# Optimization experiments

Hardware: AMD Instinct MI355X
Metric: run time of the kernel (lower is better)

## Reference

```python
import jax, jax.numpy as jnp
import numpy as np

NEG_INF = -1.0e9
LEAKY_SLOPE = 0.2


def setup_inputs() -> dict:
    key = jax.random.key(0)
    k1, k2, k3, k4, k5 = jax.random.split(key, 5)
    B, N, IN, F, H = 4, 2048, 128, 64, 4
    h = jax.random.normal(k1, (B, N, IN), dtype=jnp.float32)
    adj_matrix = jax.random.randint(k2, (B, N, N), 0, 2, dtype=jnp.int32)
    W = jax.random.normal(k3, (IN, F * H), dtype=jnp.float32) * 0.05
    a1 = jax.random.normal(k4, (F,), dtype=jnp.float32) * 0.05
    a2 = jax.random.normal(k5, (F,), dtype=jnp.float32) * 0.05
    return {"h": h, "adj_matrix": adj_matrix, "W": W, "a1": a1, "a2": a2}


def reference(h, adj_matrix, W, a1, a2):
    B, N, _ = h.shape
    F = a1.shape[0]
    H = W.shape[1] // F
    # g: [B, H, N, F]
    g = (h @ W).reshape(B, N, H, F).transpose(0, 2, 1, 3)
    # additive attention split: e[p, q] = leakyrelu(a1 . g_q + a2 . g_p)
    s_dst = jnp.einsum("bhnf,f->bhn", g, a1)  # indexed by q (column)
    s_src = jnp.einsum("bhnf,f->bhn", g, a2)  # indexed by p (row)
    e = s_src[:, :, :, None] + s_dst[:, :, None, :]  # [B,H,N,N]
    e = jnp.where(e >= 0, e, LEAKY_SLOPE * e)
    e = jnp.where(adj_matrix[:, None, :, :] == 0, NEG_INF, e)
    attention = jax.nn.softmax(e, axis=-1)  # [B,H,N,N]
    # dropout omitted (deterministic/eval reference)
    h_prime = jnp.einsum("bhpq,bhqf->bpf", attention, g) / H  # mean over heads
    return h_prime, attention.mean(axis=1)
```

## Files before the change

### kernel.cpp

```cpp
#include <hip/hip_runtime.h>
#include <stdint.h>


typedef unsigned char u8;
typedef unsigned short u16;
typedef unsigned int u32;
typedef unsigned long long u64;

typedef float f32x4 __attribute__((ext_vector_type(4)));
typedef short s16x8 __attribute__((ext_vector_type(8)));
typedef u32 u32x4 __attribute__((ext_vector_type(4)));

#define B_ 4
#define N_ 2048
#define IN_ 128
#define F_ 64
#define H_ 4
#define QS_ 8

__device__ __forceinline__ float bf2f(u16 b) {
    u32 u = ((u32)b) << 16;
    return __builtin_bit_cast(float, u);
}
__device__ __forceinline__ u16 f2bf(float f) {
    u32 u = __builtin_bit_cast(u32, f);
    u += 0x7FFFu + ((u >> 16) & 1u);
    return (u16)(u >> 16);
}

__global__ __launch_bounds__(256) void kd_detect(const u32* __restrict__ hw,
                                                 u32* __restrict__ flag) {
    __shared__ int cnt[4];
    int t = threadIdx.x;
    u32 w = hw[t];
    int e0 = (int)((w >> 7) & 0xFFu);
    int sane = (e0 >= 100 && e0 <= 145) ? 1 : 0;
#pragma unroll
    for (int m = 1; m < 64; m <<= 1) sane += __shfl_xor(sane, m, 64);
    if ((t & 63) == 0) cnt[t >> 6] = sane;
    __syncthreads();
    if (t == 0) {
        int s = cnt[0] + cnt[1] + cnt[2] + cnt[3];
        *flag = (s >= 128) ? 1u : 0u;
    }
}

__device__ __forceinline__ u16 conv_elem(const void* p, int i, u32 isbf) {
    if (isbf) return ((const u16*)p)[i];
    return f2bf(((const float*)p)[i]);
}
__global__ __launch_bounds__(256) void kc_convert(
    const void* __restrict__ h, const void* __restrict__ W, const void* __restrict__ a1,
    const void* __restrict__ a2, const u32* __restrict__ flag, u16* __restrict__ hc,
    u16* __restrict__ wt, u16* __restrict__ a1c, u16* __restrict__ a2c) {
    u32 isbf = *flag;
    int idx = blockIdx.x * 256 + threadIdx.x;
    const int NH = B_ * N_ * IN_;
    if (idx < NH) {
        hc[idx] = conv_elem(h, idx, isbf);
        return;
    }
    int j = idx - NH;
    if (j < IN_ * 256) {
        int k = j >> 8, c = j & 255;
        wt[c * IN_ + k] = conv_elem(W, j, isbf);
        return;
    }
    j -= IN_ * 256;
    if (j < F_) {
        a1c[j] = conv_elem(a1, j, isbf);
        return;
    }
    j -= F_;
    if (j < F_) a2c[j] = conv_elem(a2, j, isbf);
}

__global__ __launch_bounds__(256) void k1_proj(
    const u16* __restrict__ h, const u16* __restrict__ Wt,
    const u16* __restrict__ a1, const u16* __restrict__ a2,
    u16* __restrict__ g_f, u16* __restrict__ sdb, u32* __restrict__ e2pn,
    float* __restrict__ ssA, float2* __restrict__ ssE) {
    int b = blockIdx.x >> 7;
    int n0 = (blockIdx.x & 127) * 16;
    int w = threadIdx.x >> 6;
    int lane = threadIdx.x & 63;
    int quad = lane >> 4, l15 = lane & 15;

    f32x4 acc[4];
#pragma unroll
    for (int i = 0; i < 4; i++) acc[i] = 0.0f;

    s16x8 A[4];
#pragma unroll
    for (int kt = 0; kt < 4; kt++) {
        const s16x8* ap =
            (const s16x8*)(h + ((size_t)(b * N_ + n0 + l15) * IN_ + kt * 32 + quad * 8));
        A[kt] = *ap;
    }
#pragma unroll
    for (int kt = 0; kt < 4; kt++) {
#pragma unroll
        for (int ft = 0; ft < 4; ft++) {
            int c = w * 64 + ft * 16 + l15;
            const s16x8* bp = (const s16x8*)(Wt + ((size_t)c * IN_ + kt * 32 + quad * 8));
            acc[ft] = __builtin_amdgcn_mfma_f32_16x16x32_bf16(A[kt], *bp, acc[ft], 0, 0, 0);
        }
    }
    __shared__ float ct[4][64][20];
#pragma unroll
    for (int ft = 0; ft < 4; ft++)
#pragma unroll
        for (int r = 0; r < 4; r++) ct[w][ft * 16 + l15][quad * 4 + r] = acc[ft][r];
    __syncthreads();

    float v[16];
#pragma unroll
    for (int n = 0; n < 16; n++) v[n] = ct[w][lane][n];

    {
        int chunk = n0 >> 5;
        int gq0 = (n0 >> 3) & 2;
#pragma unroll
        for (int p = 0; p < 2; p++) {
            int ft = p * 2 + (lane >> 5);
            int lq = (lane >> 4) & 1;
            int fl = lane & 15;
            s16x8 tv;
#pragma unroll
            for (int j = 0; j < 8; j++) tv[j] = (short)f2bf(ct[w][ft * 16 + fl][lq * 8 + j]);
            size_t off =
                ((size_t)(((b * H_ + w) * 4 + ft) * 64 + chunk) * 64 + (gq0 + lq) * 16 + fl) * 8;
            *(s16x8*)(g_f + off) = tv;
        }
    }
    float a1v = bf2f(a1[lane]);
    float a2v = bf2f(a2[lane]);
    float sdv = 0.f, ssv = 0.f;
#pragma unroll
    for (int n = 0; n < 16; n++) {
        float x = v[n] * a1v;
        float y = v[n] * a2v;
#pragma unroll
        for (int m = 1; m < 64; m <<= 1) {
            x += __shfl_xor(x, m, 64);
            y += __shfl_xor(y, m, 64);
        }
        if (lane == n) { sdv = x; ssv = y; }
    }
    if (lane < 16) {
        size_t o = (size_t)(b * H_ + w) * N_ + n0 + lane;
        sdb[o] = f2bf(sdv);
        float e2p = __expf(sdv), e2n = __expf(0.2f * sdv);
        e2pn[o] = (((u32)f2bf(e2p)) << 16) | (u32)f2bf(e2n);
        ssA[o] = ssv;
        ssE[o] = make_float2(__expf(ssv), __expf(0.2f * ssv));
    }
}

__global__ __launch_bounds__(256) void k2a_rowsum(
    const int* __restrict__ adj, const u16* __restrict__ sdb, const u32* __restrict__ e2pn,
    const float* __restrict__ ssA, const float2* __restrict__ ssE,
    float2* __restrict__ E1, u32* __restrict__ pk32) {
    int b = blockIdx.x >> 9;
    int p0 = (blockIdx.x & 511) * 4;
    int t = threadIdx.x;
    int w = t >> 6, lane = t & 63;

    __shared__ u8 nib[4][512];

    float tau[4][4];
#pragma unroll
    for (int r = 0; r < 4; r++)
#pragma unroll
        for (int hh = 0; hh < 4; hh++)
            tau[r][hh] = -ssA[(size_t)(b * H_ + hh) * N_ + p0 + r];

    float S[32];
#pragma unroll
    for (int i = 0; i < 32; i++) S[i] = 0.f;

#pragma unroll
    for (int i = 0; i < 2; i++) {
        int qi = i * 256 + t;
        int q = qi * 4;
        float af[4][4];
#pragma unroll
        for (int r = 0; r < 4; r++) {
            int4 av = *(const int4*)(adj + (size_t)(b * N_ + p0 + r) * N_ + q);
            af[r][0] = (av.x != 0) ? 1.f : 0.f;
            af[r][1] = (av.y != 0) ? 1.f : 0.f;
            af[r][2] = (av.z != 0) ? 1.f : 0.f;
            af[r][3] = (av.w != 0) ? 1.f : 0.f;
            u32 nb = (av.x != 0 ? 1u : 0u) | (av.y != 0 ? 2u : 0u) |
                     (av.z != 0 ? 4u : 0u) | (av.w != 0 ? 8u : 0u);
            nib[r][qi] = (u8)nb;
        }
#pragma unroll
        for (int hh = 0; hh < 4; hh++) {
            size_t o = (size_t)(b * H_ + hh) * N_ + q;
            u64 sd4 = *(const u64*)(sdb + o);
            u32x4 pn4 = *(const u32x4*)(e2pn + o);
            float sdf[4], e2p[4], e2n[4];
#pragma unroll
            for (int j = 0; j < 4; j++) {
                sdf[j] = bf2f((u16)(sd4 >> (16 * j)));
                e2p[j] = __builtin_bit_cast(float, pn4[j] & 0xFFFF0000u);
                e2n[j] = __builtin_bit_cast(float, pn4[j] << 16);
            }
#pragma unroll
            for (int r = 0; r < 4; r++) {
#pragma unroll
                for (int j = 0; j < 4; j++) {
                    bool ge = sdf[j] >= tau[r][hh];
                    S[(r * 4 + hh) * 2 + 0] += ge ? af[r][j] * e2p[j] : 0.f;
                    S[(r * 4 + hh) * 2 + 1] += ge ? 0.f : af[r][j] * e2n[j];
                }
            }
        }
    }
    __syncthreads();
    {
        int r = t >> 6, m8 = t & 63;
        u64 nn = *(const u64*)&nib[r][m8 * 8];
        u32 wd = 0;
#pragma unroll
        for (int d = 0; d < 4; d++) {
            u32 lo = (u32)(nn >> (16 * d)) & 0xFu;
            u32 hi = (u32)(nn >> (16 * d + 8)) & 0xFu;
            wd |= (lo | (hi << 4)) << (8 * d);
        }
        pk32[(size_t)(b * N_ + p0 + r) * 64 + m8] = wd;
    }
#pragma unroll
    for (int k = 0; k < 32; k++) {
        float x = S[k];
#pragma unroll
        for (int m = 1; m < 64; m <<= 1) x += __shfl_xor(x, m, 64);
        S[k] = x;
    }
    __shared__ float sred[4][32];
    if (lane == 0) {
#pragma unroll
        for (int k = 0; k < 32; k++) sred[w][k] = S[k];
    }
    __syncthreads();
    if (t < 16) {
        int r = t >> 2, hh = t & 3;
        float sp = 0.f, sn = 0.f;
#pragma unroll
        for (int ww = 0; ww < 4; ww++) {
            sp += sred[ww][t * 2];
            sn += sred[ww][t * 2 + 1];
        }
        size_t o = (size_t)(b * H_ + hh) * N_ + p0 + r;
        float2 se = ssE[o];
        float l = se.x * sp + se.y * sn;
        float inv = (l > 0.f) ? 0.25f / l : 0.f;
        E1[o] = make_float2(se.x * inv, se.y * inv);
    }
}

__global__ __launch_bounds__(64) void k2b_attn(
    const u16* __restrict__ sdb, const u32* __restrict__ e2pn, const float* __restrict__ ssA,
    const float2* __restrict__ E1, const u32* __restrict__ pk32,
    const u16* __restrict__ g_f, const u32* __restrict__ flag, void* __restrict__ d_out_v,
    u16* __restrict__ part) {
    int bid = blockIdx.x;
    int s = bid & (QS_ - 1);
    int pt = (bid >> 3) & 127;
    int b = bid >> 10;
    int qb = s * (N_ / QS_);
    int lane = threadIdx.x;
    int quad = lane >> 4, l15 = lane & 15;
    int p0 = pt * 16;
    int row = p0 + l15;
    u32 isbf = *flag;

    __shared__ __align__(16) u16 lsd[4][256];
    __shared__ __align__(16) u32 le2[4][256];
#pragma unroll
    for (int hh = 0; hh < 4; hh++) {
        size_t o = (size_t)(b * H_ + hh) * N_ + qb + lane * 4;
        *(u64*)&lsd[hh][lane * 4] = *(const u64*)(sdb + o);
        *(u32x4*)&le2[hh][lane * 4] = *(const u32x4*)(e2pn + o);
    }
    __syncthreads();

    float E1p[4], E1n[4], tau[4];
#pragma unroll
    for (int hh = 0; hh < 4; hh++) {
        size_t o = (size_t)(b * H_ + hh) * N_ + row;
        float2 e1 = E1[o];
        E1p[hh] = e1.x;
        E1n[hh] = e1.y;
        tau[hh] = -ssA[o];
    }
    f32x4 acc[4];
#pragma unroll
    for (int i = 0; i < 4; i++) acc[i] = 0.0f;

    const u32* pkrow = pk32 + (size_t)(b * N_ + row) * 64 + (qb >> 5);
    u32 pkw[8];
#pragma unroll
    for (int c = 0; c < 8; c++) pkw[c] = pkrow[c];

    const size_t hstride = (size_t)4 * 64 * 512;
    const u16* gb = g_f + (size_t)b * H_ * hstride + (size_t)(qb >> 5) * 512 + lane * 8;

    s16x8 Bc[4], Bn[4];
#pragma unroll
    for (int ft = 0; ft < 4; ft++) Bc[ft] = *(const s16x8*)(gb + (size_t)ft * 32768);

    size_t am_base = ((size_t)(b * N_ + row)) * N_ + qb + quad * 8;
    u16* amb = (u16*)d_out_v + (size_t)B_ * N_ * F_;
    float* amf = (float*)d_out_v + (size_t)B_ * N_ * F_;

#pragma unroll 1
    for (int c = 0; c < 8; c++) {
        int qq = c * 32 + quad * 8;
        u32 byte_ = (pkw[c] >> (quad * 8)) & 0xFFu;
        float bitf[8];
#pragma unroll
        for (int j = 0; j < 8; j++) bitf[j] = ((byte_ >> j) & 1u) ? 1.0f : 0.0f;

        float amv[8];
#pragma unroll
        for (int j = 0; j < 8; j++) amv[j] = 0.f;

#pragma unroll
        for (int hh = 0; hh < 4; hh++) {
            {
                int idx = (c * 4 + hh + 1) & 31;
                int c2 = idx >> 2, h2 = idx & 3;
#pragma unroll
                for (int ft = 0; ft < 4; ft++)
                    Bn[ft] = *(const s16x8*)(gb + (size_t)h2 * hstride + (size_t)ft * 32768 +
                                             (size_t)c2 * 512);
            }
            s16x8 sd8 = *(const s16x8*)&lsd[hh][qq];
            u32x4 e2a = *(const u32x4*)&le2[hh][qq];
            u32x4 e2b = *(const u32x4*)&le2[hh][qq + 4];
            float wv[8];
#pragma unroll
            for (int j = 0; j < 8; j++) {
                float sdf = bf2f((u16)sd8[j]);
                bool ge = sdf >= tau[hh];
                u32 pn = (j < 4) ? e2a[j] : e2b[j - 4];
                float e2 = ge ? __builtin_bit_cast(float, pn & 0xFFFF0000u)
                              : __builtin_bit_cast(float, pn << 16);
                float e1v = ge ? E1p[hh] : E1n[hh];
                float ww = e1v * e2 * bitf[j];
                wv[j] = ww;
                amv[j] += ww;
            }
            s16x8 af;
#pragma unroll
            for (int j = 0; j < 8; j++) af[j] = (short)f2bf(wv[j]);
#pragma unroll
            for (int ft = 0; ft < 4; ft++)
                acc[ft] = __builtin_amdgcn_mfma_f32_16x16x32_bf16(af, Bc[ft], acc[ft], 0, 0, 0);
#pragma unroll
            for (int ft = 0; ft < 4; ft++) Bc[ft] = Bn[ft];
        }
        if (isbf) {
            s16x8 amp;
#pragma unroll
            for (int j = 0; j < 8; j++) amp[j] = (short)f2bf(amv[j]);
            *(s16x8*)(amb + am_base + c * 32) = amp;
        } else {
            f32x4 lo, hi;
#pragma unroll
            for (int j = 0; j < 4; j++) { lo[j] = amv[j]; hi[j] = amv[j + 4]; }
            *(f32x4*)(amf + am_base + c * 32) = lo;
            *(f32x4*)(amf + am_base + c * 32 + 4) = hi;
        }
    }
#pragma unroll
    for (int ft = 0; ft < 4; ft++) {
#pragma unroll
        for (int r = 0; r < 4; r++) {
            int pout = p0 + quad * 4 + r;
            int f = ft * 16 + l15;
            part[(size_t)((s * B_ + b) * N_ + pout) * F_ + f] = f2bf(acc[ft][r]);
        }
    }
}

__global__ __launch_bounds__(256) void k3_reduce(const u16* __restrict__ part,
                                                 const u32* __restrict__ flag,
                                                 void* __restrict__ out) {
    int idx = blockIdx.x * 256 + threadIdx.x;
    float s = 0.f;
#pragma unroll
    for (int i = 0; i < QS_; i++) s += bf2f(part[(size_t)i * (B_ * N_ * F_) + idx]);
    if (*flag)
        ((u16*)out)[idx] = f2bf(s);
    else
        ((float*)out)[idx] = s;
}

extern "C" void kernel_launch(void* const* d_in, const int* in_sizes, int n_in,
                              void* d_out, int out_size, void* d_ws, size_t ws_size,
                              hipStream_t stream) {
    const void* h = d_in[0];
    const int* adj = (const int*)d_in[1];
    const void* W = d_in[2];
    const void* a1 = d_in[3];
    const void* a2 = d_in[4];

    char* ws = (char*)d_ws;
    u32* flag = (u32*)(ws + 0);
    u16* a1c = (u16*)(ws + 64);
    u16* a2c = (u16*)(ws + 192);
    u16* wt = (u16*)(ws + 1024);
    u16* hc = (u16*)(ws + 66560);
    u16* g_f = (u16*)(ws + 2163712);
    u16* sdb = (u16*)(ws + 6358016);
    u32* e2pn = (u32*)(ws + 6423552);
    float* ssA = (float*)(ws + 6554624);
    float2* ssE = (float2*)(ws + 6685696);
    float2* E1 = (float2*)(ws + 6947840);
    u32* pk = (u32*)(ws + 7209984);
    u16* part = (u16*)(ws + 9307136);

    kd_detect<<<1, 256, 0, stream>>>((const u32*)h, flag);
    kc_convert<<<(B_ * N_ * IN_ + IN_ * 256 + 2 * F_ + 255) / 256, 256, 0, stream>>>(
        h, W, a1, a2, flag, hc, wt, a1c, a2c);
    k1_proj<<<512, 256, 0, stream>>>(hc, wt, a1c, a2c, g_f, sdb, e2pn, ssA, ssE);
    k2a_rowsum<<<2048, 256, 0, stream>>>(adj, sdb, e2pn, ssA, ssE, E1, pk);
    k2b_attn<<<4096, 64, 0, stream>>>(sdb, e2pn, ssA, E1, (const u32*)pk, g_f, flag,
                                      d_out, part);
    k3_reduce<<<2048, 256, 0, stream>>>(part, flag, d_out);
}
```

Before: 191.8 us.

## Double q-splits, atomically accumulate partials, fuse dtype detection into convert

Raises the q-dimension split in the attention kernel from 8 to 16, so twice as many 64-thread blocks launch, each handling half as many columns. Per-split bf16 partial buffers are replaced by float atomicAdd into one accumulator, which is zeroed inside the conversion kernel. The separate dtype-detection launch is folded into every convert block, and bf16 packing uses the paired hardware convert builtin when it exists. This aims to raise occupancy and parallelism and drop a launch, at the cost of atomic contention, a larger zeroing pass and order-dependent float summation.

```diff
diff --git a/kernel.cpp b/kernel.cpp
--- a/kernel.cpp
+++ b/kernel.cpp
@@ -16,7 +16,8 @@
 #define IN_ 128
 #define F_ 64
 #define H_ 4
-#define QS_ 8
+#define QS_ 16
+#define PARTN_ (B_ * N_ * F_)
 
 __device__ __forceinline__ float bf2f(u16 b) {
     u32 u = ((u32)b) << 16;
@@ -27,34 +28,51 @@
     u += 0x7FFFu + ((u >> 16) & 1u);
     return (u16)(u >> 16);
 }
-
-__global__ __launch_bounds__(256) void kd_detect(const u32* __restrict__ hw,
-                                                 u32* __restrict__ flag) {
-    __shared__ int cnt[4];
-    int t = threadIdx.x;
-    u32 w = hw[t];
-    int e0 = (int)((w >> 7) & 0xFFu);
-    int sane = (e0 >= 100 && e0 <= 145) ? 1 : 0;
-#pragma unroll
-    for (int m = 1; m < 64; m <<= 1) sane += __shfl_xor(sane, m, 64);
-    if ((t & 63) == 0) cnt[t >> 6] = sane;
-    __syncthreads();
-    if (t == 0) {
-        int s = cnt[0] + cnt[1] + cnt[2] + cnt[3];
-        *flag = (s >= 128) ? 1u : 0u;
-    }
+__device__ __forceinline__ u32 pk_bf16(float a, float b) {
+#if defined(__has_builtin)
+#if __has_builtin(__builtin_amdgcn_cvt_pk_bf16_f32)
+    typedef __bf16 bf2_t __attribute__((ext_vector_type(2)));
+    bf2_t p = __builtin_amdgcn_cvt_pk_bf16_f32(a, b);
+    return __builtin_bit_cast(u32, p);
+#else
+    return (u32)f2bf(a) | (((u32)f2bf(b)) << 16);
+#endif
+#else
+    return (u32)f2bf(a) | (((u32)f2bf(b)) << 16);
+#endif
 }
 
 __device__ __forceinline__ u16 conv_elem(const void* p, int i, u32 isbf) {
     if (isbf) return ((const u16*)p)[i];
     return f2bf(((const float*)p)[i]);
 }
+
 __global__ __launch_bounds__(256) void kc_convert(
     const void* __restrict__ h, const void* __restrict__ W, const void* __restrict__ a1,
-    const void* __restrict__ a2, const u32* __restrict__ flag, u16* __restrict__ hc,
-    u16* __restrict__ wt, u16* __restrict__ a1c, u16* __restrict__ a2c) {
-    u32 isbf = *flag;
-    int idx = blockIdx.x * 256 + threadIdx.x;
+    const void* __restrict__ a2, u32* __restrict__ flag, u16* __restrict__ hc,
+    u16* __restrict__ wt, u16* __restrict__ a1c, u16* __restrict__ a2c,
+    float* __restrict__ partf) {
+    __shared__ int cnt[4];
+    __shared__ u32 isbf_s;
+    int t = threadIdx.x;
+    {
+        u32 w = ((const u32*)h)[t];
+        int e0 = (int)((w >> 7) & 0xFFu);
+        int sane = (e0 >= 100 && e0 <= 145) ? 1 : 0;
+#pragma unroll
+        for (int m = 1; m < 64; m <<= 1) sane += __shfl_xor(sane, m, 64);
+        if ((t & 63) == 0) cnt[t >> 6] = sane;
+    }
+    __syncthreads();
+    if (t == 0) {
+        int s = cnt[0] + cnt[1] + cnt[2] + cnt[3];
+        isbf_s = (s >= 128) ? 1u : 0u;
+        if (blockIdx.x == 0) *flag = isbf_s;
+    }
+    __syncthreads();
+    u32 isbf = isbf_s;
+
+    int idx = blockIdx.x * 256 + t;
     const int NH = B_ * N_ * IN_;
     if (idx < NH) {
         hc[idx] = conv_elem(h, idx, isbf);
@@ -72,7 +90,12 @@
         return;
     }
     j -= F_;
-    if (j < F_) a2c[j] = conv_elem(a2, j, isbf);
+    if (j < F_) {
+        a2c[j] = conv_elem(a2, j, isbf);
+        return;
+    }
+    j -= F_;
+    if (j < PARTN_) partf[j] = 0.f;
 }
 
 __global__ __launch_bounds__(256) void k1_proj(
@@ -264,11 +287,11 @@
     const u16* __restrict__ sdb, const u32* __restrict__ e2pn, const float* __restrict__ ssA,
     const float2* __restrict__ E1, const u32* __restrict__ pk32,
     const u16* __restrict__ g_f, const u32* __restrict__ flag, void* __restrict__ d_out_v,
-    u16* __restrict__ part) {
+    float* __restrict__ partf) {
     int bid = blockIdx.x;
     int s = bid & (QS_ - 1);
-    int pt = (bid >> 3) & 127;
-    int b = bid >> 10;
+    int pt = (bid >> 4) & 127;
+    int b = bid >> 11;
     int qb = s * (N_ / QS_);
     int lane = threadIdx.x;
     int quad = lane >> 4, l15 = lane & 15;
@@ -276,13 +299,13 @@
     int row = p0 + l15;
     u32 isbf = *flag;
 
-    __shared__ __align__(16) u16 lsd[4][256];
-    __shared__ __align__(16) u32 le2[4][256];
+    __shared__ __align__(8) u16 lsd[4][128];
+    __shared__ __align__(8) u32 le2[4][128];
 #pragma unroll
     for (int hh = 0; hh < 4; hh++) {
-        size_t o = (size_t)(b * H_ + hh) * N_ + qb + lane * 4;
-        *(u64*)&lsd[hh][lane * 4] = *(const u64*)(sdb + o);
-        *(u32x4*)&le2[hh][lane * 4] = *(const u32x4*)(e2pn + o);
+        size_t o = (size_t)(b * H_ + hh) * N_ + qb + lane * 2;
+        *(u32*)&lsd[hh][lane * 2] = *(const u32*)(sdb + o);
+        *(u64*)&le2[hh][lane * 2] = *(const u64*)(e2pn + o);
     }
     __syncthreads();
 
@@ -300,9 +323,9 @@
     for (int i = 0; i < 4; i++) acc[i] = 0.0f;
 
     const u32* pkrow = pk32 + (size_t)(b * N_ + row) * 64 + (qb >> 5);
-    u32 pkw[8];
-#pragma unroll
-    for (int c = 0; c < 8; c++) pkw[c] = pkrow[c];
+    u32 pkw[4];
+#pragma unroll
+    for (int c = 0; c < 4; c++) pkw[c] = pkrow[c];
 
     const size_t hstride = (size_t)4 * 64 * 512;
     const u16* gb = g_f + (size_t)b * H_ * hstride + (size_t)(qb >> 5) * 512 + lane * 8;
@@ -316,7 +339,7 @@
     float* amf = (float*)d_out_v + (size_t)B_ * N_ * F_;
 
 #pragma unroll 1
-    for (int c = 0; c < 8; c++) {
+    for (int c = 0; c < 4; c++) {
         int qq = c * 32 + quad * 8;
         u32 byte_ = (pkw[c] >> (quad * 8)) & 0xFFu;
         float bitf[8];
@@ -330,7 +353,7 @@
 #pragma unroll
         for (int hh = 0; hh < 4; hh++) {
             {
-                int idx = (c * 4 + hh + 1) & 31;
+                int idx = (c * 4 + hh + 1) & 15;
                 int c2 = idx >> 2, h2 = idx & 3;
 #pragma unroll
                 for (int ft = 0; ft < 4; ft++)
@@ -354,8 +377,9 @@
                 amv[j] += ww;
             }
             s16x8 af;
-#pragma unroll
-            for (int j = 0; j < 8; j++) af[j] = (short)f2bf(wv[j]);
+            u32* afp = (u32*)&af;
+#pragma unroll
+            for (int j = 0; j < 4; j++) afp[j] = pk_bf16(wv[2 * j], wv[2 * j + 1]);
 #pragma unroll
             for (int ft = 0; ft < 4; ft++)
                 acc[ft] = __builtin_amdgcn_mfma_f32_16x16x32_bf16(af, Bc[ft], acc[ft], 0, 0, 0);
@@ -364,8 +388,9 @@
         }
         if (isbf) {
             s16x8 amp;
-#pragma unroll
-            for (int j = 0; j < 8; j++) amp[j] = (short)f2bf(amv[j]);
+            u32* ampp = (u32*)&amp;
+#pragma unroll
+            for (int j = 0; j < 4; j++) ampp[j] = pk_bf16(amv[2 * j], amv[2 * j + 1]);
             *(s16x8*)(amb + am_base + c * 32) = amp;
         } else {
             f32x4 lo, hi;
@@ -381,18 +406,16 @@
         for (int r = 0; r < 4; r++) {
             int pout = p0 + quad * 4 + r;
             int f = ft * 16 + l15;
-            part[(size_t)((s * B_ + b) * N_ + pout) * F_ + f] = f2bf(acc[ft][r]);
-        }
-    }
-}
-
-__global__ __launch_bounds__(256) void k3_reduce(const u16* __restrict__ part,
+            atomicAdd(&partf[(size_t)(b * N_ + pout) * F_ + f], acc[ft][r]);
+        }
+    }
+}
+
+__global__ __launch_bounds__(256) void k3_reduce(const float* __restrict__ partf,
                                                  const u32* __restrict__ flag,
                                                  void* __restrict__ out) {
     int idx = blockIdx.x * 256 + threadIdx.x;
-    float s = 0.f;
-#pragma unroll
-    for (int i = 0; i < QS_; i++) s += bf2f(part[(size_t)i * (B_ * N_ * F_) + idx]);
+    float s = partf[idx];
     if (*flag)
         ((u16*)out)[idx] = f2bf(s);
     else
@@ -421,14 +444,14 @@
     float2* ssE = (float2*)(ws + 6685696);
     float2* E1 = (float2*)(ws + 6947840);
     u32* pk = (u32*)(ws + 7209984);
-    u16* part = (u16*)(ws + 9307136);
-
-    kd_detect<<<1, 256, 0, stream>>>((const u32*)h, flag);
-    kc_convert<<<(B_ * N_ * IN_ + IN_ * 256 + 2 * F_ + 255) / 256, 256, 0, stream>>>(
-        h, W, a1, a2, flag, hc, wt, a1c, a2c);
+    float* partf = (float*)(ws + 9307136);
+
+    const int KC_TOT = B_ * N_ * IN_ + IN_ * 256 + 2 * F_ + PARTN_;
+    kc_convert<<<(KC_TOT + 255) / 256, 256, 0, stream>>>(h, W, a1, a2, flag, hc, wt, a1c,
+                                                         a2c, partf);
     k1_proj<<<512, 256, 0, stream>>>(hc, wt, a1c, a2c, g_f, sdb, e2pn, ssA, ssE);
     k2a_rowsum<<<2048, 256, 0, stream>>>(adj, sdb, e2pn, ssA, ssE, E1, pk);
-    k2b_attn<<<4096, 64, 0, stream>>>(sdb, e2pn, ssA, E1, (const u32*)pk, g_f, flag,
-                                      d_out, part);
-    k3_reduce<<<2048, 256, 0, stream>>>(part, flag, d_out);
-}
+    k2b_attn<<<8192, 64, 0, stream>>>(sdb, e2pn, ssA, E1, (const u32*)pk, g_f, flag,
+                                      d_out, partf);
+    k3_reduce<<<2048, 256, 0, stream>>>(partf, flag, d_out);
+}
```

After: 196.9 us. +2.6%, slower.
